# Kernel tuning notes

Hardware: AMD Instinct MI355X
Metric: run time of the kernel (lower is better)

## Reference

```python
import jax, jax.numpy as jnp
import numpy as np

NEG = -10000.0


def _build_label_vocab():
    vocab = {'O': 0}
    i = 1
    for t in ['PER', 'ORG', 'LOC', 'MISC']:
        for p in ['B', 'I', 'E', 'S']:
            vocab[f'{p}-{t}'] = i
            i += 1
    return vocab


def _init_transition(key):
    """Random transition with BIOES constraints, matching CRF.initialize()."""
    vocab = _build_label_vocab()
    L = len(vocab) + 2          # 19 (17 labels + start + end)
    start, end = L - 2, L - 1
    T = np.array(jax.random.normal(key, (L, L)), dtype=np.float32)
    T[:, end] = NEG
    T[start, :] = NEG
    for lf, i_f in vocab.items():
        pf, tf = ('O', 'O') if lf == 'O' else lf.split('-')
        for lt, i_t in vocab.items():
            pt, tt = ('O', 'O') if lt == 'O' else lt.split('-')
            allowed = (pf in ('O', 'E', 'S') and pt in ('O', 'B', 'S')) or \
                      (pf in ('B', 'I') and pt in ('I', 'E') and tf == tt)
            if not allowed:
                T[i_t, i_f] = NEG
    return jnp.asarray(T)


def setup_inputs() -> dict:
    key = jax.random.key(0)
    k1, k2, k3, k4 = jax.random.split(key, 4)
    B, S, NL = 4096, 256, 17
    logits = jax.random.normal(k1, (B, S, NL), dtype=jnp.float32)
    labels = jax.random.randint(k2, (B, S), 0, NL)
    lens = jax.random.randint(k3, (B,), 1, S + 1)   # lengths in [1, S]
    transition = _init_transition(k4)                # [19, 19]
    return {"logits": logits, "labels": labels, "lens": lens,
            "transition": transition}


def reference(logits, labels, lens, transition):
    """CRF log-likelihood: gold_score(pad_logits(logits)) - norm_score."""
    B, S, NL = logits.shape
    L = transition.shape[0]       # label_size = NL + 2
    start, end = L - 2, L - 1

    # pad_logits: append start/end columns with -10000
    pads = jnp.full((B, S, 2), NEG, dtype=logits.dtype)
    logits_p = jnp.concatenate([logits, pads], axis=2)   # [B, S, L]

    tmask = (jnp.arange(S)[None, :] < lens[:, None])     # [B, S] valid tokens

    # ---- gold score ----
    # unary: gather emission score of the gold label at each position
    unary = jnp.take_along_axis(logits_p, labels[:, :, None], axis=2)[:, :, 0]
    unary = (unary * tmask.astype(logits.dtype)).sum(axis=1)

    # binary: transition scores along the gold path (with start/end padding)
    labels_ext = jnp.concatenate(
        [jnp.full((B, 1), start, labels.dtype), labels,
         jnp.full((B, 1), end, labels.dtype)], axis=1)   # [B, S+2]
    emask = jnp.arange(S + 2)[None, :] < (lens + 1)[:, None]
    labels_ext = jnp.where(emask, labels_ext, end)
    trn_scr = transition[labels_ext[:, 1:], labels_ext[:, :-1]]  # [B, S+1]
    bmask = (jnp.arange(S + 1)[None, :] < (lens + 1)[:, None]).astype(logits.dtype)
    binary = (trn_scr * bmask).sum(axis=1)

    gold = unary + binary

    # ---- partition (norm) score: forward algorithm over time ----
    alpha0 = jnp.full((B, L), NEG, dtype=logits.dtype).at[:, start].set(0.0)

    def step(alpha, xs):
        logit, m = xs  # logit: [B, L], m: [B] bool (position < len)
        # alpha_nxt[b,i] = logit[b,i] + LSE_j(alpha[b,j] + T[i,j])
        nxt = logit + jax.nn.logsumexp(alpha[:, None, :] + transition[None], axis=2)
        alpha = jnp.where(m[:, None], nxt, alpha)
        return alpha, None

    alpha, _ = jax.lax.scan(step, alpha0,
                            (jnp.swapaxes(logits_p, 0, 1), tmask.T))
    alpha = alpha + transition[end][None, :]
    norm = jax.nn.logsumexp(alpha, axis=1)

    return gold - norm   # [B] per-sequence log-likelihood
```

## Files before the change

kernel.cpp:

```cpp
#include <hip/hip_runtime.h>

constexpr int S  = 256;
constexpr int NL = 17;
constexpr int L  = 19;
constexpr int WPB = 2;

__global__ __launch_bounds__(64 * WPB)
void crf_fwd(const float* __restrict__ logits,
             const int*   __restrict__ labels,
             const int*   __restrict__ lens,
             const float* __restrict__ transition,
             float* __restrict__ out)
{
    __shared__ float Tsh[L * L];
    __shared__ __align__(16) float pbuf[WPB][2][2][20];

    const int tid  = threadIdx.x;
    const int wave = tid >> 6;
    const int wtid = tid & 63;
    const int half = wtid >> 5;
    const int lane = wtid & 31;
    const int b    = blockIdx.x * WPB + wave;

    for (int k = tid; k < L * L; k += 64 * WPB) Tsh[k] = transition[k];
    __syncthreads();

    const int  i   = lane;
    const bool act = (i < L);
    const int  ic  = act ? i : 0;

    float coef[L];
    #pragma unroll
    for (int j = 0; j < L; ++j)
        coef[j] = __expf(half ? Tsh[j * L + ic] : Tsh[ic * L + j]);

    const int len = lens[b];
    const int mid = len >> 1;
    const int nf  = mid;
    const int nb  = len - mid;
    const int nup = half ? nb : nf;
    const int nsteps8 = (nb + 7) & ~7;

    const float* lgp  = logits + (size_t)b * S * NL;
    const int*   labp = labels + (size_t)b * S;

    float p = half ? (act ? __expf(Tsh[(L - 1) * L + ic]) : 0.0f)
                   : ((i == L - 2) ? 1.0f : 0.0f);
    float m    = 0.0f;
    float utot = 0.0f;
    float btot = 0.0f;
    int   prevF = L - 2;

    if (half) btot = Tsh[(L - 1) * L + labp[len - 1]];

    float lgbuf[8];
    int   labbuf[8];
    #pragma unroll
    for (int u = 0; u < 8; ++u) {
        int tb0 = len - 1 - u; tb0 = (tb0 > 0) ? tb0 : 0;
        const int tok = half ? tb0 : u;
        lgbuf[u]  = (i < NL) ? lgp[tok * NL + i] : 0.0f;
        labbuf[u] = labp[tok];
    }

    for (int tb = 0; tb < nsteps8; tb += 8) {
        #pragma unroll
        for (int u = 0; u < 8; ++u) {
            const int   t   = tb + u;
            const float lg  = lgbuf[u];
            const int   lab = labbuf[u];
            const int   labnxt = labbuf[(u + 1) & 7];
            {
                int tpf = t + 8;       tpf = (tpf < S) ? tpf : (S - 1);
                int tpb = len - 9 - t; tpb = (tpb > 0) ? tpb : 0;
                const int tok = half ? tpb : tpf;
                lgbuf[u]  = (i < NL) ? lgp[tok * NL + i] : 0.0f;
                labbuf[u] = labp[tok];
            }
            const bool upd = (t < nup);

            int prv;
            if (half) {
                const int utok = len - 1 - t;
                prv = (utok >= 1) ? labnxt : (L - 2);
            } else {
                prv = prevF;
            }
            utot += (upd && i == lab) ? lg : 0.0f;
            const float gtr = Tsh[lab * L + prv];
            btot += upd ? gtr : 0.0f;
            prevF = upd ? lab : prevF;

            const float el = (i < NL) ? __expf(lg) : 0.0f;
            const float pe = p * el;
            const float wv = half ? pe : p;

            float* pb = &pbuf[wave][half][u & 1][0];
            if (act) pb[i] = wv;
            asm volatile("s_waitcnt lgkmcnt(0)" ::: "memory");
            const float4* q = (const float4*)pb;
            const float4 q0 = q[0], q1 = q[1], q2 = q[2], q3 = q[3], q4 = q[4];

            float a0 = q0.x * coef[0];
            float a1 = q0.y * coef[1];
            float a2 = q0.z * coef[2];
            float a3 = q0.w * coef[3];
            a0 = fmaf(q1.x, coef[4],  a0);
            a1 = fmaf(q1.y, coef[5],  a1);
            a2 = fmaf(q1.z, coef[6],  a2);
            a3 = fmaf(q1.w, coef[7],  a3);
            a0 = fmaf(q2.x, coef[8],  a0);
            a1 = fmaf(q2.y, coef[9],  a1);
            a2 = fmaf(q2.z, coef[10], a2);
            a3 = fmaf(q2.w, coef[11], a3);
            a0 = fmaf(q3.x, coef[12], a0);
            a1 = fmaf(q3.y, coef[13], a1);
            a2 = fmaf(q3.z, coef[14], a2);
            a3 = fmaf(q3.w, coef[15], a3);
            a0 = fmaf(q4.x, coef[16], a0);
            a1 = fmaf(q4.y, coef[17], a1);
            a2 = fmaf(q4.z, coef[18], a2);

            const float v   = (a0 + a1) + (a2 + a3);
            const float elf = half ? 1.0f : el;
            float pn = v * elf;

            if ((t & 3) == 3) {
                float m0 = fmaxf(fmaxf(q0.x, q0.y), fmaxf(q0.z, q0.w));
                float m1 = fmaxf(fmaxf(q1.x, q1.y), fmaxf(q1.z, q1.w));
                float m2 = fmaxf(fmaxf(q2.x, q2.y), fmaxf(q2.z, q2.w));
                float m3 = fmaxf(fmaxf(q3.x, q3.y), fmaxf(q3.z, q3.w));
                float m4 = fmaxf(fmaxf(q4.x, q4.y), q4.z);
                float mx = fmaxf(fmaxf(m0, m1), fmaxf(fmaxf(m2, m3), m4));
                pn *= __frcp_rn(mx);
                if (upd) m += __logf(mx);
            }
            p = upd ? pn : p;
        }
    }

    const float other = __shfl_xor(p, 32);
    float prod = act ? p * other : 0.0f;
    #pragma unroll
    for (int off = 16; off >= 1; off >>= 1)
        prod += __shfl_xor(prod, off, 32);
    const float mtot = m + __shfl_xor(m, 32);
    const float norm = mtot + __logf(prod);

    #pragma unroll
    for (int off = 16; off >= 1; off >>= 1)
        utot += __shfl_xor(utot, off, 32);
    const float ghalf = utot + btot;
    const float gold  = ghalf + __shfl_xor(ghalf, 32);

    if (wtid == 0) out[b] = gold - norm;
}

extern "C" void kernel_launch(void* const* d_in, const int* in_sizes, int n_in,
                              void* d_out, int out_size, void* d_ws, size_t ws_size,
                              hipStream_t stream)
{
    (void)n_in; (void)out_size; (void)d_ws; (void)ws_size;
    const float* logits     = (const float*)d_in[0];
    const int*   labels     = (const int*)d_in[1];
    const int*   lens       = (const int*)d_in[2];
    const float* transition = (const float*)d_in[3];
    float*       out        = (float*)d_out;
    const int B = in_sizes[2];
    crf_fwd<<<dim3(B / WPB), dim3(64 * WPB), 0, stream>>>(logits, labels, lens, transition, out);
}
```

Measured before the change: 140.4 us.

## Move gold-path scoring out of recurrence and streamline bidirectional forward loop

Removes the per-step gold unary/binary score accumulation and label loads from the serial forward/backward recurrence and computes the gold score afterwards in one parallel pass over tokens across all 64 lanes. The meeting point is rebalanced so both halves run mid steps: the forward half folds the start transition into its initial vector, and the backward half applies the final emission once after the loop. Logit prefetch now uses clamped byte offsets with a fixed stride instead of recomputing token indices each step. This shortens the latency-bound per-step critical path, at the cost of an extra epilogue pass and more index-clamping logic.

```diff
diff --git a/kernel.cpp b/kernel.cpp
--- a/kernel.cpp
+++ b/kernel.cpp
@@ -1,8 +1,8 @@
 #include <hip/hip_runtime.h>
 
-constexpr int S  = 256;
-constexpr int NL = 17;
-constexpr int L  = 19;
+constexpr int S   = 256;
+constexpr int NL  = 17;
+constexpr int L   = 19;
 constexpr int WPB = 2;
 
 __global__ __launch_bounds__(64 * WPB)
@@ -10,10 +10,10 @@
              const int*   __restrict__ labels,
              const int*   __restrict__ lens,
              const float* __restrict__ transition,
-             float* __restrict__ out)
+             float* __restrict__ out, int totalElemM1)
 {
     __shared__ float Tsh[L * L];
-    __shared__ __align__(16) float pbuf[WPB][2][2][20];
+    __shared__ __align__(16) float pbuf[WPB][2][2][32];
 
     const int tid  = threadIdx.x;
     const int wave = tid >> 6;
@@ -25,9 +25,10 @@
     for (int k = tid; k < L * L; k += 64 * WPB) Tsh[k] = transition[k];
     __syncthreads();
 
-    const int  i   = lane;
-    const bool act = (i < L);
-    const int  ic  = act ? i : 0;
+    const int  i    = lane;
+    const bool act  = (i < L);
+    const bool emit = (i < NL);
+    const int  ic   = act ? i : 0;
 
     float coef[L];
     #pragma unroll
@@ -36,67 +37,53 @@
 
     const int len = lens[b];
     const int mid = len >> 1;
-    const int nf  = mid;
-    const int nb  = len - mid;
-    const int nup = half ? nb : nf;
-    const int nsteps8 = (nb + 7) & ~7;
+    const int nb  = len - 1 - mid;
+    const int nup = half ? nb : mid;
+    const int nsteps = (mid + 7) & ~7;
 
-    const float* lgp  = logits + (size_t)b * S * NL;
-    const int*   labp = labels + (size_t)b * S;
+    const int seqbase = b * (S * NL);
 
-    float p = half ? (act ? __expf(Tsh[(L - 1) * L + ic]) : 0.0f)
-                   : ((i == L - 2) ? 1.0f : 0.0f);
-    float m    = 0.0f;
-    float utot = 0.0f;
-    float btot = 0.0f;
-    int   prevF = L - 2;
+    float p = act ? __expf(half ? Tsh[(L - 1) * L + ic]
+                                : Tsh[ic * L + (L - 2)])
+                  : 0.0f;
+    float m = 0.0f;
 
-    if (half) btot = Tsh[(L - 1) * L + labp[len - 1]];
+    const char* lgbase = (const char*)logits;
+    const int capHiF = 4 * min(seqbase + (S - 1) * NL + i, totalElemM1);
+    const int capHi  = half ? 0x7ffffffc : capHiF;
+    const int capLo  = half ? 4 * (seqbase + i) : 0;
+    const int stride = half ? -(8 * NL * 4) : (8 * NL * 4);
 
+    int   off[8];
     float lgbuf[8];
-    int   labbuf[8];
     #pragma unroll
     for (int u = 0; u < 8; ++u) {
-        int tb0 = len - 1 - u; tb0 = (tb0 > 0) ? tb0 : 0;
-        const int tok = half ? tb0 : u;
-        lgbuf[u]  = (i < NL) ? lgp[tok * NL + i] : 0.0f;
-        labbuf[u] = labp[tok];
+        int tok = half ? (len - 1 - u) : u;
+        tok = tok > 0 ? tok : 0;
+        int o = 4 * (seqbase + tok * NL + i);
+        o = min(o, capHiF);
+        off[u] = o;
+        lgbuf[u] = *(const float*)(lgbase + o);
     }
 
-    for (int tb = 0; tb < nsteps8; tb += 8) {
+    for (int tb = 0; tb < nsteps; tb += 8) {
         #pragma unroll
         for (int u = 0; u < 8; ++u) {
-            const int   t   = tb + u;
-            const float lg  = lgbuf[u];
-            const int   lab = labbuf[u];
-            const int   labnxt = labbuf[(u + 1) & 7];
-            {
-                int tpf = t + 8;       tpf = (tpf < S) ? tpf : (S - 1);
-                int tpb = len - 9 - t; tpb = (tpb > 0) ? tpb : 0;
-                const int tok = half ? tpb : tpf;
-                lgbuf[u]  = (i < NL) ? lgp[tok * NL + i] : 0.0f;
-                labbuf[u] = labp[tok];
-            }
+            const int   t  = tb + u;
+            const float lg = lgbuf[u];
+            int o = off[u] + stride;
+            o = max(o, capLo);
+            o = min(o, capHi);
+            off[u] = o;
+            lgbuf[u] = *(const float*)(lgbase + o);
+
             const bool upd = (t < nup);
 
-            int prv;
-            if (half) {
-                const int utok = len - 1 - t;
-                prv = (utok >= 1) ? labnxt : (L - 2);
-            } else {
-                prv = prevF;
-            }
-            utot += (upd && i == lab) ? lg : 0.0f;
-            const float gtr = Tsh[lab * L + prv];
-            btot += upd ? gtr : 0.0f;
-            prevF = upd ? lab : prevF;
-
-            const float el = (i < NL) ? __expf(lg) : 0.0f;
+            const float el = emit ? __expf(lg) : 0.0f;
             const float pe = p * el;
-            const float wv = half ? pe : p;
 
             float* pb = &pbuf[wave][half][u & 1][0];
-            if (act) pb[i] = wv;
+            pb[i] = pe;
             asm volatile("s_waitcnt lgkmcnt(0)" ::: "memory");
             const float4* q = (const float4*)pb;
             const float4 q0 = q[0], q1 = q[1], q2 = q[2], q3 = q[3], q4 = q[4];
@@ -121,11 +108,9 @@
             a1 = fmaf(q4.y, coef[17], a1);
             a2 = fmaf(q4.z, coef[18], a2);
 
-            const float v   = (a0 + a1) + (a2 + a3);
-            const float elf = half ? 1.0f : el;
-            float pn = v * elf;
+            float pn = (a0 + a1) + (a2 + a3);
 
-            if ((t & 3) == 3) {
+            if ((u & 3) == 3) {
                 float m0 = fmaxf(fmaxf(q0.x, q0.y), fmaxf(q0.z, q0.w));
                 float m1 = fmaxf(fmaxf(q1.x, q1.y), fmaxf(q1.z, q1.w));
                 float m2 = fmaxf(fmaxf(q2.x, q2.y), fmaxf(q2.z, q2.w));
@@ -133,25 +118,38 @@
                 float m4 = fmaxf(fmaxf(q4.x, q4.y), q4.z);
                 float mx = fmaxf(fmaxf(m0, m1), fmaxf(fmaxf(m2, m3), m4));
                 pn *= __frcp_rn(mx);
-                if (upd) m += __logf(mx);
+                m += upd ? __logf(mx) : 0.0f;
             }
             p = upd ? pn : p;
         }
     }
 
+    {
+        float lgf = 0.0f;
+        if (half && emit) lgf = logits[(size_t)(seqbase + mid * NL + i)];
+        if (half) p = emit ? p * __expf(lgf) : 0.0f;
+    }
+
     const float other = __shfl_xor(p, 32);
     float prod = act ? p * other : 0.0f;
     #pragma unroll
-    for (int off = 16; off >= 1; off >>= 1)
-        prod += __shfl_xor(prod, off, 32);
+    for (int o = 16; o >= 1; o >>= 1) prod += __shfl_xor(prod, o, 32);
     const float mtot = m + __shfl_xor(m, 32);
     const float norm = mtot + __logf(prod);
 
+    const int* labp = labels + b * S;
+    float gsum = 0.0f;
+    for (int c = 0; c < len; c += 64) {
+        const int tok = c + wtid;
+        if (tok < len) {
+            const int lab = labp[tok];
+            const int prv = (tok == 0) ? (L - 2) : labp[tok - 1];
+            gsum += logits[(size_t)(seqbase + tok * NL + lab)] + Tsh[lab * L + prv];
+        }
+    }
     #pragma unroll
-    for (int off = 16; off >= 1; off >>= 1)
-        utot += __shfl_xor(utot, off, 32);
-    const float ghalf = utot + btot;
-    const float gold  = ghalf + __shfl_xor(ghalf, 32);
+    for (int o = 32; o >= 1; o >>= 1) gsum += __shfl_xor(gsum, o);
+    const float gold = gsum + Tsh[(L - 1) * L + labp[len - 1]];
 
     if (wtid == 0) out[b] = gold - norm;
 }
@@ -167,5 +165,7 @@
     const float* transition = (const float*)d_in[3];
     float*       out        = (float*)d_out;
     const int B = in_sizes[2];
-    crf_fwd<<<dim3(B / WPB), dim3(64 * WPB), 0, stream>>>(logits, labels, lens, transition, out);
+    const int totalElemM1 = B * S * NL - 1;
+    crf_fwd<<<dim3(B / WPB), dim3(64 * WPB), 0, stream>>>(
+        logits, labels, lens, transition, out, totalElemM1);
 }
```

Result: faster. 137.1 us (-2.3%).
